# Kernel optimization log

Measured on AMD Instinct MI355X. Metric: run time of the kernel, lower is better.

## Reference

```python
import jax, jax.numpy as jnp
import numpy as np

IN_FEATURES = 4096
OUT_FEATURES = 4096
RANKS = (1, 16, 16, 1)
M_IN = 16   # in_core_features, 16**3 == 4096
M_OUT = 16  # out_core_features
ORDER = 3


def setup_inputs() -> dict:
    key = jax.random.key(0)
    k_x, k0, k1, k2, kb = jax.random.split(key, 5)
    s = 0.05
    x = jax.random.normal(k_x, (2, 1024, IN_FEATURES), dtype=jnp.float32)
    core0 = jax.random.normal(k0, (RANKS[0], M_IN, M_OUT, RANKS[1]), dtype=jnp.float32) * s
    core1 = jax.random.normal(k1, (RANKS[1], M_IN, M_OUT, RANKS[2]), dtype=jnp.float32) * s
    core2 = jax.random.normal(k2, (RANKS[2], M_IN, M_OUT, RANKS[3]), dtype=jnp.float32) * s
    bound = 1.0 / np.sqrt(IN_FEATURES)
    bias = jax.random.uniform(kb, (OUT_FEATURES,), dtype=jnp.float32,
                              minval=-bound, maxval=bound)
    return {"x": x, "core0": core0, "core1": core1, "core2": core2, "bias": bias}


def reference(x, core0, core1, core2, bias):
    lead_shape = x.shape[:-1]
    pad = M_IN ** ORDER - IN_FEATURES  # 0 here, kept for generality
    xf = x.reshape(-1, IN_FEATURES)
    if pad:
        xf = jnp.pad(xf, ((0, 0), (0, pad)))
    t = xf.reshape(-1, M_IN, M_IN, M_IN)                 # [b, i1, i2, i3]
    # TT core chain contraction (cores: [r_i, i, o, r_{i+1}])
    t = jnp.einsum('bijk,pixq->bjkxq', t, core0)          # sum i1, r0 -> [b, i2, i3, o1, r1]
    t = jnp.einsum('bjkxq,qjyr->bkxyr', t, core1)         # sum i2, r1 -> [b, i3, o1, o2, r2]
    t = jnp.einsum('bkxyr,rkzs->bxyzs', t, core2)         # sum i3, r2 -> [b, o1, o2, o3, 1]
    out = t.reshape(t.shape[0], -1)[:, :OUT_FEATURES]     # truncate padded output dims
    out = out.reshape(*lead_shape, OUT_FEATURES) + bias
    return out
```

## Files before the change

kernel.cpp:

```cpp
#include <hip/hip_runtime.h>
#include <hip/hip_bf16.h>

typedef unsigned short ushort_t;
typedef __attribute__((ext_vector_type(4))) float f32x4;
typedef __attribute__((ext_vector_type(8))) short bf16x8;
typedef __attribute__((ext_vector_type(8))) unsigned short u16x8;

#define M_DIM 2048
#define N_DIM 4096
#define K_DIM 4096
#define BM 256
#define BN 128
#define BK 64
#define NT (K_DIM / BK)

#define MFMA16(a, b, c) __builtin_amdgcn_mfma_f32_16x16x32_bf16((a), (b), (c), 0, 0, 0)

__device__ __forceinline__ unsigned short f2bf(float f) {
  unsigned int u = __float_as_uint(f);
  u += 0x7FFFu + ((u >> 16) & 1u);
  return (unsigned short)(u >> 16);
}

__device__ __forceinline__ void async16(void* l, const void* g) {
  __builtin_amdgcn_global_load_lds(
      (const __attribute__((address_space(1))) void*)g,
      (__attribute__((address_space(3))) void*)l,
      16, 0, 0);
}

__global__ void k_prep(const float* __restrict__ x, ushort_t* __restrict__ o,
                       const float* __restrict__ c0, const float* __restrict__ c1,
                       const float* __restrict__ c2, ushort_t* __restrict__ wt) {
  __shared__ float sc1[16 * 260];
  const int bid = blockIdx.x;
  const int tid = threadIdx.x;
  if (bid < 2048) {
    const int n4 = (M_DIM * K_DIM) / 4;
    for (int i = bid * 256 + tid; i < n4; i += 2048 * 256) {
      float4 v = ((const float4*)x)[i];
      ushort4 r;
      r.x = f2bf(v.x); r.y = f2bf(v.y); r.z = f2bf(v.z); r.w = f2bf(v.w);
      ((ushort4*)o)[i] = r;
    }
  } else {
    const int out = bid - 2048;
    const int o3 = out & 15;
    const int o2 = (out >> 4) & 15;
    const int o1 = out >> 8;

    {
      const int q  = tid >> 4;
      const int i2 = tid & 15;
      const float* src = c1 + q * 4096 + i2 * 256 + o2 * 16;
      float* dst = &sc1[i2 * 260 + q * 16];
      #pragma unroll
      for (int rr = 0; rr < 4; ++rr)
        *(float4*)(dst + rr * 4) = *(const float4*)(src + rr * 4);
    }
    __syncthreads();

    const int i2 = tid & 15;
    const int i1 = tid >> 4;

    float4 a4[4];
    {
      const float* c0p = c0 + (i1 * 16 + o1) * 16;
      #pragma unroll
      for (int rr = 0; rr < 4; ++rr) a4[rr] = *(const float4*)(c0p + rr * 4);
    }

    float t01r[16];
    #pragma unroll
    for (int r = 0; r < 16; ++r) t01r[r] = 0.f;
    #pragma unroll
    for (int q = 0; q < 16; ++q) {
      const float a = a4[q >> 2][q & 3];
      const float* sp = &sc1[i2 * 260 + q * 16];
      #pragma unroll
      for (int rr = 0; rr < 4; ++rr) {
        float4 v = *(const float4*)(sp + rr * 4);
        t01r[rr * 4 + 0] += a * v.x;
        t01r[rr * 4 + 1] += a * v.y;
        t01r[rr * 4 + 2] += a * v.z;
        t01r[rr * 4 + 3] += a * v.w;
      }
    }

    u16x8 lo, hi;
    #pragma unroll
    for (int i3 = 0; i3 < 16; ++i3) {
      const float* c2p = c2 + i3 * 16 + o3;
      float s = 0.f;
      #pragma unroll
      for (int rr = 0; rr < 16; ++rr) s += t01r[rr] * c2p[rr * 256];
      ushort_t v = f2bf(s);
      if (i3 < 8) lo[i3] = v; else hi[i3 - 8] = v;
    }
    u16x8* dst = (u16x8*)(wt + ((size_t)out << 12) + (i1 << 8) + (i2 << 4));
    dst[0] = lo;
    dst[1] = hi;
  }
}

__global__ __launch_bounds__(512, 2) void k_gemm(
    const ushort_t* __restrict__ A,
    const ushort_t* __restrict__ Bt,
    const float* __restrict__ bias,
    float* __restrict__ C)
{
  __shared__ ushort_t lA[3][BM * BK];
  __shared__ ushort_t lB[3][BN * BK];

  const int tid  = threadIdx.x;
  const int lane = tid & 63;
  const int wid  = tid >> 6;
  const int wm   = wid >> 1;
  const int wn   = wid & 1;
  const int fr   = lane & 15;
  const int fg   = lane >> 4;

  const int bid = blockIdx.x;
  const int bm  = bid & 7;
  const int bn  = bid >> 3;

  const int srow = tid >> 3;
  const int scol = ((tid & 7) ^ (srow & 7)) << 3;
  const ushort_t* aSt = A  + (size_t)(bm * BM + srow) * K_DIM + scol;
  const ushort_t* bSt = Bt + (size_t)(bn * BN + srow) * K_DIM + scol;
  const int dE = tid * 8;

#define STAGE_A(kt, s, r_) async16(&lA[s][(r_) * 4096 + dE], \
                                   aSt + (size_t)(kt) * BK + (size_t)(r_) * 64 * K_DIM)
#define STAGE_B(kt, s, r_) async16(&lB[s][(r_) * 4096 + dE], \
                                   bSt + (size_t)(kt) * BK + (size_t)(r_) * 64 * K_DIM)

  const int arowb = wm * 64 + fr;
  const int browb = wn * 64 + fr;
  const int c0 = ( fg      ^ (fr & 7)) << 3;
  const int c1 = ((fg + 4) ^ (fr & 7)) << 3;

  f32x4 acc[4][4];
  #pragma unroll
  for (int m = 0; m < 4; ++m)
    #pragma unroll
    for (int n = 0; n < 4; ++n)
      acc[m][n] = (f32x4){0.f, 0.f, 0.f, 0.f};

  #pragma unroll
  for (int r_ = 0; r_ < 4; ++r_) STAGE_A(0, 0, r_);
  #pragma unroll
  for (int r_ = 0; r_ < 2; ++r_) STAGE_B(0, 0, r_);
  #pragma unroll
  for (int r_ = 0; r_ < 4; ++r_) STAGE_A(1, 1, r_);
  #pragma unroll
  for (int r_ = 0; r_ < 2; ++r_) STAGE_B(1, 1, r_);

  asm volatile("s_waitcnt vmcnt(6)" ::: "memory");
  __builtin_amdgcn_s_barrier();

  int sc = 0, ss = 2;
  for (int t = 0; t < NT; ++t) {
    const bool pre = (t + 2 < NT);
    const ushort_t* pA = &lA[sc][0];
    const ushort_t* pB = &lB[sc][0];

    {
      bf16x8 af[4], bf[4];
      #pragma unroll
      for (int m = 0; m < 4; ++m) af[m] = *(const bf16x8*)(pA + (arowb + m * 16) * 64 + c0);
      #pragma unroll
      for (int n = 0; n < 4; ++n) bf[n] = *(const bf16x8*)(pB + (browb + n * 16) * 64 + c0);
      if (pre) { STAGE_A(t + 2, ss, 0); STAGE_A(t + 2, ss, 1); STAGE_A(t + 2, ss, 2); }
      __builtin_amdgcn_s_barrier();
      __builtin_amdgcn_s_setprio(1);
      #pragma unroll
      for (int m = 0; m < 4; ++m)
        #pragma unroll
        for (int n = 0; n < 4; ++n)
          acc[m][n] = MFMA16(af[m], bf[n], acc[m][n]);
      __builtin_amdgcn_s_setprio(0);
      __builtin_amdgcn_s_barrier();
    }

    {
      bf16x8 af[4], bf[4];
      #pragma unroll
      for (int m = 0; m < 4; ++m) af[m] = *(const bf16x8*)(pA + (arowb + m * 16) * 64 + c1);
      #pragma unroll
      for (int n = 0; n < 4; ++n) bf[n] = *(const bf16x8*)(pB + (browb + n * 16) * 64 + c1);
      if (pre) { STAGE_A(t + 2, ss, 3); STAGE_B(t + 2, ss, 0); STAGE_B(t + 2, ss, 1); }
      __builtin_amdgcn_s_barrier();
      __builtin_amdgcn_s_setprio(1);
      #pragma unroll
      for (int m = 0; m < 4; ++m)
        #pragma unroll
        for (int n = 0; n < 4; ++n)
          acc[m][n] = MFMA16(af[m], bf[n], acc[m][n]);
      __builtin_amdgcn_s_setprio(0);
      if (t + 2 < NT)      asm volatile("s_waitcnt vmcnt(6)" ::: "memory");
      else if (t + 1 < NT) asm volatile("s_waitcnt vmcnt(0)" ::: "memory");
      __builtin_amdgcn_s_barrier();
    }

    sc = (sc == 2) ? 0 : sc + 1;
    ss = (ss == 2) ? 0 : ss + 1;
  }
#undef STAGE_A
#undef STAGE_B

  const size_t row0 = (size_t)bm * BM + wm * 64;
  const int col0 = bn * BN + wn * 64;
  #pragma unroll
  for (int n = 0; n < 4; ++n) {
    const int col = col0 + n * 16 + fr;
    const float bv = bias[col];
    #pragma unroll
    for (int m = 0; m < 4; ++m) {
      const size_t r0 = row0 + m * 16 + fg * 4;
      #pragma unroll
      for (int r = 0; r < 4; ++r)
        C[(r0 + r) * N_DIM + col] = acc[m][n][r] + bv;
    }
  }
}

extern "C" void kernel_launch(void* const* d_in, const int* in_sizes, int n_in,
                              void* d_out, int out_size, void* d_ws, size_t ws_size,
                              hipStream_t stream) {
  const float* x    = (const float*)d_in[0];
  const float* c0   = (const float*)d_in[1];
  const float* c1   = (const float*)d_in[2];
  const float* c2   = (const float*)d_in[3];
  const float* bias = (const float*)d_in[4];
  float* out = (float*)d_out;

  const size_t NEED = (size_t)48 * 1024 * 1024;
  if (ws_size < NEED) return;

  char* ws = (char*)d_ws;
  ushort_t* Abf = (ushort_t*)ws;
  ushort_t* Wt  = (ushort_t*)(ws + (size_t)16 * 1024 * 1024);

  k_prep <<<6144, 256, 0, stream>>>(x, Abf, c0, c1, c2, Wt);
  k_gemm <<<256, 512, 0, stream>>>(Abf, Wt, bias, out);
}
```

Baseline: 106.6 us.

## Load A operand directly from global into registers, bypassing LDS staging

The GEMM no longer stages the A tile through shared memory. Each wave now loads its A fragments straight from global memory into a double-buffered register set, prefetching the next k-tile while the current one computes. Only B still goes through the triple-buffered async LDS pipeline, and the loop now has one barrier per k-tile instead of several. This cuts LDS traffic and footprint and removes synchronisation, but A is fetched redundantly by both N-waves and with less coalesced access. The tighter vmcnt waits may also expose global latency.

```diff
diff --git a/kernel.cpp b/kernel.cpp
--- a/kernel.cpp
+++ b/kernel.cpp
@@ -109,7 +109,6 @@
     const float* __restrict__ bias,
     float* __restrict__ C)
 {
-  __shared__ ushort_t lA[3][BM * BK];
   __shared__ ushort_t lB[3][BN * BK];
 
   const int tid  = threadIdx.x;
@@ -126,19 +125,25 @@
 
   const int srow = tid >> 3;
   const int scol = ((tid & 7) ^ (srow & 7)) << 3;
-  const ushort_t* aSt = A  + (size_t)(bm * BM + srow) * K_DIM + scol;
   const ushort_t* bSt = Bt + (size_t)(bn * BN + srow) * K_DIM + scol;
   const int dE = tid * 8;
 
-#define STAGE_A(kt, s, r_) async16(&lA[s][(r_) * 4096 + dE], \
-                                   aSt + (size_t)(kt) * BK + (size_t)(r_) * 64 * K_DIM)
 #define STAGE_B(kt, s, r_) async16(&lB[s][(r_) * 4096 + dE], \
                                    bSt + (size_t)(kt) * BK + (size_t)(r_) * 64 * K_DIM)
 
-  const int arowb = wm * 64 + fr;
   const int browb = wn * 64 + fr;
-  const int c0 = ( fg      ^ (fr & 7)) << 3;
-  const int c1 = ((fg + 4) ^ (fr & 7)) << 3;
+  const int cc0 = ( fg      ^ (fr & 7)) << 3;
+  const int cc1 = ((fg + 4) ^ (fr & 7)) << 3;
+
+  const ushort_t* aBase = A + (size_t)(bm * BM + wm * 64 + fr) * K_DIM + fg * 8;
+
+#define LOADA(dst, kt) do {                                                          \
+    _Pragma("unroll")                                                                \
+    for (int m_ = 0; m_ < 4; ++m_) {                                                 \
+      dst[m_][0] = *(const bf16x8*)(aBase + (size_t)m_ * 16 * K_DIM + (kt) * 64);    \
+      dst[m_][1] = *(const bf16x8*)(aBase + (size_t)m_ * 16 * K_DIM + (kt) * 64 + 32);\
+    }                                                                                \
+  } while (0)
 
   f32x4 acc[4][4];
   #pragma unroll
@@ -147,66 +152,54 @@
     for (int n = 0; n < 4; ++n)
       acc[m][n] = (f32x4){0.f, 0.f, 0.f, 0.f};
 
-  #pragma unroll
-  for (int r_ = 0; r_ < 4; ++r_) STAGE_A(0, 0, r_);
-  #pragma unroll
-  for (int r_ = 0; r_ < 2; ++r_) STAGE_B(0, 0, r_);
-  #pragma unroll
-  for (int r_ = 0; r_ < 4; ++r_) STAGE_A(1, 1, r_);
-  #pragma unroll
-  for (int r_ = 0; r_ < 2; ++r_) STAGE_B(1, 1, r_);
-
-  asm volatile("s_waitcnt vmcnt(6)" ::: "memory");
+  bf16x8 aE[4][2], aO[4][2];
+
+  STAGE_B(0, 0, 0); STAGE_B(0, 0, 1);
+  STAGE_B(1, 1, 0); STAGE_B(1, 1, 1);
+  LOADA(aE, 0);
+  asm volatile("s_waitcnt vmcnt(8)" ::: "memory");
   __builtin_amdgcn_s_barrier();
 
   int sc = 0, ss = 2;
-  for (int t = 0; t < NT; ++t) {
-    const bool pre = (t + 2 < NT);
-    const ushort_t* pA = &lA[sc][0];
-    const ushort_t* pB = &lB[sc][0];
-
-    {
-      bf16x8 af[4], bf[4];
-      #pragma unroll
-      for (int m = 0; m < 4; ++m) af[m] = *(const bf16x8*)(pA + (arowb + m * 16) * 64 + c0);
-      #pragma unroll
-      for (int n = 0; n < 4; ++n) bf[n] = *(const bf16x8*)(pB + (browb + n * 16) * 64 + c0);
-      if (pre) { STAGE_A(t + 2, ss, 0); STAGE_A(t + 2, ss, 1); STAGE_A(t + 2, ss, 2); }
-      __builtin_amdgcn_s_barrier();
-      __builtin_amdgcn_s_setprio(1);
-      #pragma unroll
-      for (int m = 0; m < 4; ++m)
-        #pragma unroll
-        for (int n = 0; n < 4; ++n)
-          acc[m][n] = MFMA16(af[m], bf[n], acc[m][n]);
-      __builtin_amdgcn_s_setprio(0);
-      __builtin_amdgcn_s_barrier();
-    }
-
-    {
-      bf16x8 af[4], bf[4];
-      #pragma unroll
-      for (int m = 0; m < 4; ++m) af[m] = *(const bf16x8*)(pA + (arowb + m * 16) * 64 + c1);
-      #pragma unroll
-      for (int n = 0; n < 4; ++n) bf[n] = *(const bf16x8*)(pB + (browb + n * 16) * 64 + c1);
-      if (pre) { STAGE_A(t + 2, ss, 3); STAGE_B(t + 2, ss, 0); STAGE_B(t + 2, ss, 1); }
-      __builtin_amdgcn_s_barrier();
-      __builtin_amdgcn_s_setprio(1);
-      #pragma unroll
-      for (int m = 0; m < 4; ++m)
-        #pragma unroll
-        for (int n = 0; n < 4; ++n)
-          acc[m][n] = MFMA16(af[m], bf[n], acc[m][n]);
-      __builtin_amdgcn_s_setprio(0);
-      if (t + 2 < NT)      asm volatile("s_waitcnt vmcnt(6)" ::: "memory");
-      else if (t + 1 < NT) asm volatile("s_waitcnt vmcnt(0)" ::: "memory");
-      __builtin_amdgcn_s_barrier();
-    }
-
-    sc = (sc == 2) ? 0 : sc + 1;
-    ss = (ss == 2) ? 0 : ss + 1;
+
+#define BODY(t, aCur, aNxt) do {                                                  \
+    const bool pre_ = ((t) + 2 < NT);                                             \
+    const ushort_t* pB_ = &lB[sc][0];                                             \
+    if (pre_) { STAGE_B((t) + 2, ss, 0); STAGE_B((t) + 2, ss, 1); }               \
+    bf16x8 bf0_[4], bf1_[4];                                                      \
+    _Pragma("unroll")                                                             \
+    for (int n_ = 0; n_ < 4; ++n_)                                                \
+      bf0_[n_] = *(const bf16x8*)(pB_ + (browb + n_ * 16) * 64 + cc0);            \
+    _Pragma("unroll")                                                             \
+    for (int n_ = 0; n_ < 4; ++n_)                                                \
+      bf1_[n_] = *(const bf16x8*)(pB_ + (browb + n_ * 16) * 64 + cc1);            \
+    { const int ktn_ = ((t) + 1 < NT) ? (t) + 1 : (t);                            \
+      LOADA(aNxt, ktn_); }                                                        \
+    __builtin_amdgcn_s_setprio(1);                                                \
+    _Pragma("unroll")                                                             \
+    for (int m_ = 0; m_ < 4; ++m_)                                                \
+      _Pragma("unroll")                                                           \
+      for (int n_ = 0; n_ < 4; ++n_)                                              \
+        acc[m_][n_] = MFMA16(aCur[m_][0], bf0_[n_], acc[m_][n_]);                 \
+    _Pragma("unroll")                                                             \
+    for (int m_ = 0; m_ < 4; ++m_)                                                \
+      _Pragma("unroll")                                                           \
+      for (int n_ = 0; n_ < 4; ++n_)                                              \
+        acc[m_][n_] = MFMA16(aCur[m_][1], bf1_[n_], acc[m_][n_]);                 \
+    __builtin_amdgcn_s_setprio(0);                                                \
+     \
+    asm volatile("s_waitcnt vmcnt(8)" ::: "memory");                              \
+    __builtin_amdgcn_s_barrier();                                                 \
+    sc = (sc == 2) ? 0 : sc + 1;                                                  \
+    ss = (ss == 2) ? 0 : ss + 1;                                                  \
+  } while (0)
+
+  for (int it = 0; it < NT / 2; ++it) {
+    BODY(2 * it,     aE, aO);
+    BODY(2 * it + 1, aO, aE);
   }
-#undef STAGE_A
+#undef BODY
+#undef LOADA
 #undef STAGE_B
 
   const size_t row0 = (size_t)bm * BM + wm * 64;
```

Measured after the change: 183.0 us. +71.6%, slower.

## Double-buffer LDS fragments in registers and cut per-iteration barriers to one

Applied to the files above, without the earlier changes.

The GEMM main loop now holds the next K-half's A/B fragments in registers (cur/nxt). LDS reads for the following tile are issued while the MFMAs for the current half run. The four barriers per K-tile drop to one, with all four A stage copies and the B stage copies regrouped around the MFMA blocks. This is meant to hide LDS read latency and cut synchronization stalls. In exchange it uses more VGPRs, which could press the 2-block occupancy target, and the correctness of buffer reuse depends on careful vmcnt and barrier placement.

```diff
diff --git a/kernel.cpp b/kernel.cpp
--- a/kernel.cpp
+++ b/kernel.cpp
@@ -137,8 +137,8 @@
 
   const int arowb = wm * 64 + fr;
   const int browb = wn * 64 + fr;
-  const int c0 = ( fg      ^ (fr & 7)) << 3;
-  const int c1 = ((fg + 4) ^ (fr & 7)) << 3;
+  const int cc0 = ( fg      ^ (fr & 7)) << 3;
+  const int cc1 = ((fg + 4) ^ (fr & 7)) << 3;
 
   f32x4 acc[4][4];
   #pragma unroll
@@ -158,6 +158,12 @@
 
   asm volatile("s_waitcnt vmcnt(6)" ::: "memory");
   __builtin_amdgcn_s_barrier();
+
+  bf16x8 curA[4], curB[4], nxtA[4], nxtB[4];
+  #pragma unroll
+  for (int m = 0; m < 4; ++m) curA[m] = *(const bf16x8*)(&lA[0][0] + (arowb + m * 16) * 64 + cc0);
+  #pragma unroll
+  for (int n = 0; n < 4; ++n) curB[n] = *(const bf16x8*)(&lB[0][0] + (browb + n * 16) * 64 + cc0);
 
   int sc = 0, ss = 2;
   for (int t = 0; t < NT; ++t) {
@@ -165,43 +171,49 @@
     const ushort_t* pA = &lA[sc][0];
     const ushort_t* pB = &lB[sc][0];
 
-    {
-      bf16x8 af[4], bf[4];
-      #pragma unroll
-      for (int m = 0; m < 4; ++m) af[m] = *(const bf16x8*)(pA + (arowb + m * 16) * 64 + c0);
-      #pragma unroll
-      for (int n = 0; n < 4; ++n) bf[n] = *(const bf16x8*)(pB + (browb + n * 16) * 64 + c0);
-      if (pre) { STAGE_A(t + 2, ss, 0); STAGE_A(t + 2, ss, 1); STAGE_A(t + 2, ss, 2); }
-      __builtin_amdgcn_s_barrier();
-      __builtin_amdgcn_s_setprio(1);
-      #pragma unroll
-      for (int m = 0; m < 4; ++m)
-        #pragma unroll
-        for (int n = 0; n < 4; ++n)
-          acc[m][n] = MFMA16(af[m], bf[n], acc[m][n]);
-      __builtin_amdgcn_s_setprio(0);
-      __builtin_amdgcn_s_barrier();
-    }
-
-    {
-      bf16x8 af[4], bf[4];
-      #pragma unroll
-      for (int m = 0; m < 4; ++m) af[m] = *(const bf16x8*)(pA + (arowb + m * 16) * 64 + c1);
-      #pragma unroll
-      for (int n = 0; n < 4; ++n) bf[n] = *(const bf16x8*)(pB + (browb + n * 16) * 64 + c1);
-      if (pre) { STAGE_A(t + 2, ss, 3); STAGE_B(t + 2, ss, 0); STAGE_B(t + 2, ss, 1); }
-      __builtin_amdgcn_s_barrier();
-      __builtin_amdgcn_s_setprio(1);
-      #pragma unroll
-      for (int m = 0; m < 4; ++m)
-        #pragma unroll
-        for (int n = 0; n < 4; ++n)
-          acc[m][n] = MFMA16(af[m], bf[n], acc[m][n]);
-      __builtin_amdgcn_s_setprio(0);
-      if (t + 2 < NT)      asm volatile("s_waitcnt vmcnt(6)" ::: "memory");
-      else if (t + 1 < NT) asm volatile("s_waitcnt vmcnt(0)" ::: "memory");
-      __builtin_amdgcn_s_barrier();
-    }
+    #pragma unroll
+    for (int m = 0; m < 4; ++m) nxtA[m] = *(const bf16x8*)(pA + (arowb + m * 16) * 64 + cc1);
+    #pragma unroll
+    for (int n = 0; n < 4; ++n) nxtB[n] = *(const bf16x8*)(pB + (browb + n * 16) * 64 + cc1);
+
+    if (pre) { STAGE_A(t + 2, ss, 0); STAGE_A(t + 2, ss, 1);
+               STAGE_A(t + 2, ss, 2); STAGE_A(t + 2, ss, 3); }
+
+    __builtin_amdgcn_s_setprio(1);
+    #pragma unroll
+    for (int m = 0; m < 4; ++m)
+      #pragma unroll
+      for (int n = 0; n < 4; ++n)
+        acc[m][n] = MFMA16(curA[m], curB[n], acc[m][n]);
+    __builtin_amdgcn_s_setprio(0);
+
+    if (t + 1 < NT) {
+      if (t == NT - 2) {
+        asm volatile("s_waitcnt vmcnt(0)" ::: "memory");
+        __builtin_amdgcn_s_barrier();
+      }
+      const int sn = (sc == 2) ? 0 : sc + 1;
+      const ushort_t* qA = &lA[sn][0];
+      const ushort_t* qB = &lB[sn][0];
+      #pragma unroll
+      for (int m = 0; m < 4; ++m) curA[m] = *(const bf16x8*)(qA + (arowb + m * 16) * 64 + cc0);
+      #pragma unroll
+      for (int n = 0; n < 4; ++n) curB[n] = *(const bf16x8*)(qB + (browb + n * 16) * 64 + cc0);
+    }
+
+    if (pre) { STAGE_B(t + 2, ss, 0); STAGE_B(t + 2, ss, 1); }
+
+    __builtin_amdgcn_s_setprio(1);
+    #pragma unroll
+    for (int m = 0; m < 4; ++m)
+      #pragma unroll
+      for (int n = 0; n < 4; ++n)
+        acc[m][n] = MFMA16(nxtA[m], nxtB[n], acc[m][n]);
+    __builtin_amdgcn_s_setprio(0);
+
+    if (t + 2 < NT)      asm volatile("s_waitcnt vmcnt(6)" ::: "memory");
+    else                 asm volatile("s_waitcnt vmcnt(0)" ::: "memory");
+    __builtin_amdgcn_s_barrier();
 
     sc = (sc == 2) ? 0 : sc + 1;
     ss = (ss == 2) ? 0 : ss + 1;
```

Result: slower. 109.2 us (+2.4%).

## Restructure GEMM to 128x256 tiles with 4 waves and XCD-aware block mapping

Applied to the files above, without the earlier changes.

Switches the GEMM block tile from 256x128 with 8 waves to 128x256 with 4 waves. Each wave now owns the full 128 rows and a 64-column slice, so it holds 8x4 accumulator tiles. Block IDs are remapped so that blocks on the same XCD share A and B panels, which should improve L2 reuse. The per-half-tile barriers are cut down to one barrier per K-step, with a matching vmcnt wait. The trade-off is fewer waves per CU and higher register pressure from 32 accumulators per wave, which reduces latency hiding.

```diff
diff --git a/kernel.cpp b/kernel.cpp
--- a/kernel.cpp
+++ b/kernel.cpp
@@ -9,8 +9,8 @@
 #define M_DIM 2048
 #define N_DIM 4096
 #define K_DIM 4096
-#define BM 256
-#define BN 128
+#define BM 128
+#define BN 256
 #define BK 64
 #define NT (K_DIM / BK)
 
@@ -103,7 +103,7 @@
   }
 }
 
-__global__ __launch_bounds__(512, 2) void k_gemm(
+__global__ __launch_bounds__(256, 1) void k_gemm(
     const ushort_t* __restrict__ A,
     const ushort_t* __restrict__ Bt,
     const float* __restrict__ bias,
@@ -115,14 +115,14 @@
   const int tid  = threadIdx.x;
   const int lane = tid & 63;
   const int wid  = tid >> 6;
-  const int wm   = wid >> 1;
-  const int wn   = wid & 1;
   const int fr   = lane & 15;
   const int fg   = lane >> 4;
 
   const int bid = blockIdx.x;
-  const int bm  = bid & 7;
-  const int bn  = bid >> 3;
+  const int xcd = bid & 7;
+  const int l   = bid >> 3;
+  const int bm  = (xcd & 1) * 8 + (l & 7);
+  const int bn  = (xcd >> 1) * 4 + (l >> 3);
 
   const int srow = tid >> 3;
   const int scol = ((tid & 7) ^ (srow & 7)) << 3;
@@ -130,19 +130,18 @@
   const ushort_t* bSt = Bt + (size_t)(bn * BN + srow) * K_DIM + scol;
   const int dE = tid * 8;
 
-#define STAGE_A(kt, s, r_) async16(&lA[s][(r_) * 4096 + dE], \
-                                   aSt + (size_t)(kt) * BK + (size_t)(r_) * 64 * K_DIM)
-#define STAGE_B(kt, s, r_) async16(&lB[s][(r_) * 4096 + dE], \
-                                   bSt + (size_t)(kt) * BK + (size_t)(r_) * 64 * K_DIM)
-
-  const int arowb = wm * 64 + fr;
-  const int browb = wn * 64 + fr;
-  const int c0 = ( fg      ^ (fr & 7)) << 3;
-  const int c1 = ((fg + 4) ^ (fr & 7)) << 3;
-
-  f32x4 acc[4][4];
-  #pragma unroll
-  for (int m = 0; m < 4; ++m)
+#define STAGE_A(kt, s, r_) async16(&lA[s][(r_) * 2048 + dE], \
+                                   aSt + (size_t)(kt) * BK + (size_t)(r_) * 32 * K_DIM)
+#define STAGE_B(kt, s, r_) async16(&lB[s][(r_) * 2048 + dE], \
+                                   bSt + (size_t)(kt) * BK + (size_t)(r_) * 32 * K_DIM)
+
+  const int browb = wid * 64 + fr;
+  const int cc0 = ( fg      ^ (fr & 7)) << 3;
+  const int cc1 = ((fg + 4) ^ (fr & 7)) << 3;
+
+  f32x4 acc[8][4];
+  #pragma unroll
+  for (int m = 0; m < 8; ++m)
     #pragma unroll
     for (int n = 0; n < 4; ++n)
       acc[m][n] = (f32x4){0.f, 0.f, 0.f, 0.f};
@@ -150,13 +149,13 @@
   #pragma unroll
   for (int r_ = 0; r_ < 4; ++r_) STAGE_A(0, 0, r_);
   #pragma unroll
-  for (int r_ = 0; r_ < 2; ++r_) STAGE_B(0, 0, r_);
+  for (int r_ = 0; r_ < 8; ++r_) STAGE_B(0, 0, r_);
   #pragma unroll
   for (int r_ = 0; r_ < 4; ++r_) STAGE_A(1, 1, r_);
   #pragma unroll
-  for (int r_ = 0; r_ < 2; ++r_) STAGE_B(1, 1, r_);
-
-  asm volatile("s_waitcnt vmcnt(6)" ::: "memory");
+  for (int r_ = 0; r_ < 8; ++r_) STAGE_B(1, 1, r_);
+
+  asm volatile("s_waitcnt vmcnt(12)" ::: "memory");
   __builtin_amdgcn_s_barrier();
 
   int sc = 0, ss = 2;
@@ -166,42 +165,48 @@
     const ushort_t* pB = &lB[sc][0];
 
     {
-      bf16x8 af[4], bf[4];
-      #pragma unroll
-      for (int m = 0; m < 4; ++m) af[m] = *(const bf16x8*)(pA + (arowb + m * 16) * 64 + c0);
-      #pragma unroll
-      for (int n = 0; n < 4; ++n) bf[n] = *(const bf16x8*)(pB + (browb + n * 16) * 64 + c0);
-      if (pre) { STAGE_A(t + 2, ss, 0); STAGE_A(t + 2, ss, 1); STAGE_A(t + 2, ss, 2); }
-      __builtin_amdgcn_s_barrier();
+      bf16x8 af[8], bf[4];
+      #pragma unroll
+      for (int m = 0; m < 8; ++m) af[m] = *(const bf16x8*)(pA + (m * 16 + fr) * 64 + cc0);
+      #pragma unroll
+      for (int n = 0; n < 4; ++n) bf[n] = *(const bf16x8*)(pB + (browb + n * 16) * 64 + cc0);
+      if (pre) {
+        STAGE_A(t + 2, ss, 0); STAGE_A(t + 2, ss, 1);
+        STAGE_A(t + 2, ss, 2); STAGE_A(t + 2, ss, 3);
+        STAGE_B(t + 2, ss, 0); STAGE_B(t + 2, ss, 1);
+      }
       __builtin_amdgcn_s_setprio(1);
       #pragma unroll
-      for (int m = 0; m < 4; ++m)
+      for (int m = 0; m < 8; ++m)
         #pragma unroll
         for (int n = 0; n < 4; ++n)
           acc[m][n] = MFMA16(af[m], bf[n], acc[m][n]);
       __builtin_amdgcn_s_setprio(0);
-      __builtin_amdgcn_s_barrier();
-    }
-
-    {
-      bf16x8 af[4], bf[4];
-      #pragma unroll
-      for (int m = 0; m < 4; ++m) af[m] = *(const bf16x8*)(pA + (arowb + m * 16) * 64 + c1);
-      #pragma unroll
-      for (int n = 0; n < 4; ++n) bf[n] = *(const bf16x8*)(pB + (browb + n * 16) * 64 + c1);
-      if (pre) { STAGE_A(t + 2, ss, 3); STAGE_B(t + 2, ss, 0); STAGE_B(t + 2, ss, 1); }
-      __builtin_amdgcn_s_barrier();
+    }
+
+    {
+      bf16x8 af[8], bf[4];
+      #pragma unroll
+      for (int m = 0; m < 8; ++m) af[m] = *(const bf16x8*)(pA + (m * 16 + fr) * 64 + cc1);
+      #pragma unroll
+      for (int n = 0; n < 4; ++n) bf[n] = *(const bf16x8*)(pB + (browb + n * 16) * 64 + cc1);
+      if (pre) {
+        STAGE_B(t + 2, ss, 2); STAGE_B(t + 2, ss, 3);
+        STAGE_B(t + 2, ss, 4); STAGE_B(t + 2, ss, 5);
+        STAGE_B(t + 2, ss, 6); STAGE_B(t + 2, ss, 7);
+      }
       __builtin_amdgcn_s_setprio(1);
       #pragma unroll
-      for (int m = 0; m < 4; ++m)
+      for (int m = 0; m < 8; ++m)
         #pragma unroll
         for (int n = 0; n < 4; ++n)
           acc[m][n] = MFMA16(af[m], bf[n], acc[m][n]);
       __builtin_amdgcn_s_setprio(0);
-      if (t + 2 < NT)      asm volatile("s_waitcnt vmcnt(6)" ::: "memory");
-      else if (t + 1 < NT) asm volatile("s_waitcnt vmcnt(0)" ::: "memory");
-      __builtin_amdgcn_s_barrier();
-    }
+    }
+
+    if (pre) asm volatile("s_waitcnt vmcnt(12)" ::: "memory");
+    else     asm volatile("s_waitcnt vmcnt(0)"  ::: "memory");
+    __builtin_amdgcn_s_barrier();
 
     sc = (sc == 2) ? 0 : sc + 1;
     ss = (ss == 2) ? 0 : ss + 1;
@@ -209,14 +214,14 @@
 #undef STAGE_A
 #undef STAGE_B
 
-  const size_t row0 = (size_t)bm * BM + wm * 64;
-  const int col0 = bn * BN + wn * 64;
+  const size_t row0 = (size_t)bm * BM;
+  const int col0 = bn * BN + wid * 64;
   #pragma unroll
   for (int n = 0; n < 4; ++n) {
     const int col = col0 + n * 16 + fr;
     const float bv = bias[col];
     #pragma unroll
-    for (int m = 0; m < 4; ++m) {
+    for (int m = 0; m < 8; ++m) {
       const size_t r0 = row0 + m * 16 + fg * 4;
       #pragma unroll
       for (int r = 0; r < 4; ++r)
@@ -243,5 +248,5 @@
   ushort_t* Wt  = (ushort_t*)(ws + (size_t)16 * 1024 * 1024);
 
   k_prep <<<6144, 256, 0, stream>>>(x, Abf, c0, c1, c2, Wt);
-  k_gemm <<<256, 512, 0, stream>>>(Abf, Wt, bias, out);
-}
+  k_gemm <<<256, 256, 0, stream>>>(Abf, Wt, bias, out);
+}
```

Result: no change. 108.3 us (+1.5%).
